# Optimization experiments

Hardware: AMD Instinct MI355X
Metric: run time of the kernel (lower is better)

Reference implementation:

```python
import jax, jax.numpy as jnp
import numpy as np

BLOCK = 128          # quantization block size
F8_MAX = 448.0       # max representable magnitude of float8_e4m3fn


def setup_inputs() -> dict:
    key = jax.random.key(0)
    k1, k2, k3 = jax.random.split(key, 3)
    M, K, N = 8192, 4096, 4096
    Kb, Nb = K // BLOCK, N // BLOCK
    x = jax.random.normal(k1, (M, K), jnp.float32)
    # weight stored as fp8-representable values (simulated with f32 container)
    weight = jax.random.normal(k2, (N, K), jnp.float32)
    # per 128x128-block weight dequant scales (positive, small, like amax/448)
    weight_scale = jax.random.uniform(k3, (Nb, Kb), jnp.float32, 0.5, 1.5) * 0.01
    return {"x": x, "weight": weight, "weight_scale": weight_scale}


def _act_quant(x):
    """fp8_blockwise_act_quant: per-(row, 128-block) scale = amax/448, cast to e4m3."""
    M, K = x.shape
    Kb = K // BLOCK
    xb = x.reshape(M, Kb, BLOCK)
    amax = jnp.max(jnp.abs(xb), axis=-1, keepdims=True)            # [M, Kb, 1]
    scale = jnp.maximum(amax, 1e-12) / F8_MAX                      # [M, Kb, 1]
    xq = (xb / scale).astype(jnp.float8_e4m3fn).astype(jnp.float32)
    return xq, scale


def reference(x, weight, weight_scale):
    # ---- activation blockwise fp8 quant ----
    xq, x_scale = _act_quant(x)                                    # [M,Kb,B], [M,Kb,1]
    M, Kb, _ = xq.shape
    K = Kb * BLOCK
    x_deq = (xq * x_scale).reshape(M, K)                           # dequantized activations

    # ---- weight blockwise fp8 dequant (weight stored as fp8 values) ----
    N = weight.shape[0]
    Nb = N // BLOCK
    wq = weight.astype(jnp.float8_e4m3fn).astype(jnp.float32)      # fp8 storage
    w_deq = (wq.reshape(Nb, BLOCK, Kb, BLOCK)
             * weight_scale[:, None, :, None]).reshape(N, K)

    # ---- scaled GEMM: y = x_deq @ w_deq^T (bias is None) ----
    return x_deq @ w_deq.T                                         # [M, N]
```

## Files before the change

### kernel.cpp

```cpp
#include <hip/hip_runtime.h>


typedef int   v4i __attribute__((ext_vector_type(4)));
typedef int   v8i __attribute__((ext_vector_type(8)));
typedef float v4f __attribute__((ext_vector_type(4)));

constexpr int M  = 8192;
constexpr int K  = 4096;
constexpr int N  = 4096;
constexpr int KB = K / 128;
constexpr int NB = N / 128;

#define GLOBAL_AS __attribute__((address_space(1)))
#define LDS_AS    __attribute__((address_space(3)))

__device__ __forceinline__ void async16(const void* g, void* l) {
  __builtin_amdgcn_global_load_lds((const GLOBAL_AS void*)g, (LDS_AS void*)l, 16, 0, 0);
}


__global__ __launch_bounds__(256) void quant_x_kernel(
    const float* __restrict__ x, unsigned char* __restrict__ xq,
    float* __restrict__ xs_t ) {
  const int tid = threadIdx.x;
  const long long blk = ((long long)blockIdx.x * 256 + tid) >> 3;
  const int s = tid & 7;
  const int m  = (int)(blk >> 5);
  const int kb = (int)(blk & (KB - 1));

  const float4* px = (const float4*)(x + blk * 128 + s * 16);
  float4 v0 = px[0], v1 = px[1], v2 = px[2], v3 = px[3];

  float ax = 0.f;
#define AMAX4(v) ax = fmaxf(ax, fmaxf(fmaxf(fabsf(v.x), fabsf(v.y)), fmaxf(fabsf(v.z), fabsf(v.w))))
  AMAX4(v0); AMAX4(v1); AMAX4(v2); AMAX4(v3);
#undef AMAX4
#pragma unroll
  for (int d = 4; d >= 1; d >>= 1) ax = fmaxf(ax, __shfl_xor(ax, d, 8));
  const float scale = fmaxf(ax, 1e-12f) / 448.0f;

  int p0 = 0, p1 = 0, p2 = 0, p3 = 0;
  p0 = __builtin_amdgcn_cvt_pk_fp8_f32(v0.x / scale, v0.y / scale, p0, false);
  p0 = __builtin_amdgcn_cvt_pk_fp8_f32(v0.z / scale, v0.w / scale, p0, true);
  p1 = __builtin_amdgcn_cvt_pk_fp8_f32(v1.x / scale, v1.y / scale, p1, false);
  p1 = __builtin_amdgcn_cvt_pk_fp8_f32(v1.z / scale, v1.w / scale, p1, true);
  p2 = __builtin_amdgcn_cvt_pk_fp8_f32(v2.x / scale, v2.y / scale, p2, false);
  p2 = __builtin_amdgcn_cvt_pk_fp8_f32(v2.z / scale, v2.w / scale, p2, true);
  p3 = __builtin_amdgcn_cvt_pk_fp8_f32(v3.x / scale, v3.y / scale, p3, false);
  p3 = __builtin_amdgcn_cvt_pk_fp8_f32(v3.z / scale, v3.w / scale, p3, true);

  const int q = s >> 1, j = s & 1, rr = m & 15;
  const long long base = ((long long)(m >> 4) * KB + kb) * 2048;
  *(v4i*)(xq + base + j * 1024 + (q * 16 + rr) * 16) = (v4i){p0, p1, p2, p3};

  if (s == 0) xs_t[(long long)kb * M + m] = scale;
}

__global__ __launch_bounds__(256) void quant_w_kernel(
    const float* __restrict__ w, unsigned char* __restrict__ wq) {
  const long long t = (long long)blockIdx.x * 256 + threadIdx.x;
  const int grp = (int)(t >> 7);
  const int idx = (int)(t & 127);
  const int l = idx >> 1, j = idx & 1;
  const int nf = grp >> 5, kb = grp & (KB - 1);
  const int n = nf * 16 + (l & 15);
  const int k = kb * 128 + (l >> 4) * 32 + j * 16;

  const float4* pw = (const float4*)(w + (long long)n * K + k);
  float4 v0 = pw[0], v1 = pw[1], v2 = pw[2], v3 = pw[3];
  int p0 = 0, p1 = 0, p2 = 0, p3 = 0;
  p0 = __builtin_amdgcn_cvt_pk_fp8_f32(v0.x, v0.y, p0, false);
  p0 = __builtin_amdgcn_cvt_pk_fp8_f32(v0.z, v0.w, p0, true);
  p1 = __builtin_amdgcn_cvt_pk_fp8_f32(v1.x, v1.y, p1, false);
  p1 = __builtin_amdgcn_cvt_pk_fp8_f32(v1.z, v1.w, p1, true);
  p2 = __builtin_amdgcn_cvt_pk_fp8_f32(v2.x, v2.y, p2, false);
  p2 = __builtin_amdgcn_cvt_pk_fp8_f32(v2.z, v2.w, p2, true);
  p3 = __builtin_amdgcn_cvt_pk_fp8_f32(v3.x, v3.y, p3, false);
  p3 = __builtin_amdgcn_cvt_pk_fp8_f32(v3.z, v3.w, p3, true);
  *(v4i*)(wq + (long long)grp * 2048 + j * 1024 + l * 16) = (v4i){p0, p1, p2, p3};
}

__global__ __launch_bounds__(256, 2) void gemm_fp8_kernel(
    const unsigned char* __restrict__ xq, const unsigned char* __restrict__ wq,
    const float* __restrict__ xs_t ,
    const float* __restrict__ wscale ,
    float* __restrict__ out) {
  __shared__ unsigned char Asm[16 * 2048];
  __shared__ unsigned char Bsm[8 * 2048];
  __shared__ float Stab[KB * 256];

  const int tid   = threadIdx.x;
  const int ntile = blockIdx.x;
  const int mtile = blockIdx.y;
  const int wave  = tid >> 6;
  const int lane  = tid & 63;
  const int wm = wave >> 1, wn = wave & 1;
  const int l15 = lane & 15, quad = lane >> 4;

  for (int i = tid; i < KB * 256; i += 256) {
    const int kb = i >> 8, r = i & 255;
    Stab[i] = xs_t[(long long)kb * M + mtile * 256 + r] * wscale[ntile * KB + kb];
  }

  const unsigned char* pa0 =
      xq + ((long long)(mtile * 16 + wave * 4) * KB) * 2048 + lane * 16;
  const unsigned char* pb0 =
      wq + ((long long)(ntile * 8 + wave * 2) * KB) * 2048 + lane * 16;
  const int a_lds0 = wave * 4 * 2048;
  const int b_lds0 = wave * 2 * 2048;

  v4f acc[8][4];
#pragma unroll
  for (int f = 0; f < 8; ++f)
#pragma unroll
    for (int g = 0; g < 4; ++g) acc[f][g] = (v4f){0.f, 0.f, 0.f, 0.f};

  const v4f z = (v4f){0.f, 0.f, 0.f, 0.f};

#pragma unroll 1
  for (int kb = 0; kb < KB; ++kb) {
    const long long koff = (long long)kb * 2048;
#pragma unroll
    for (int t = 0; t < 8; ++t)
      async16(pa0 + koff + (long long)(t >> 1) * (KB * 2048) + (t & 1) * 1024,
              Asm + a_lds0 + (t >> 1) * 2048 + (t & 1) * 1024);
#pragma unroll
    for (int t = 0; t < 4; ++t)
      async16(pb0 + koff + (long long)(t >> 1) * (KB * 2048) + (t & 1) * 1024,
              Bsm + b_lds0 + (t >> 1) * 2048 + (t & 1) * 1024);
    __syncthreads();

    v8i b[4];
#pragma unroll
    for (int g = 0; g < 4; ++g) {
      const unsigned char* pb = Bsm + (wn * 4 + g) * 2048 + lane * 16;
      v4i lo = *(const v4i*)pb;
      v4i hi = *(const v4i*)(pb + 1024);
      b[g][0] = lo[0]; b[g][1] = lo[1]; b[g][2] = lo[2]; b[g][3] = lo[3];
      b[g][4] = hi[0]; b[g][5] = hi[1]; b[g][6] = hi[2]; b[g][7] = hi[3];
    }

#pragma unroll
    for (int f = 0; f < 8; ++f) {
      const unsigned char* pa = Asm + (wm * 8 + f) * 2048 + lane * 16;
      v4i lo = *(const v4i*)pa;
      v4i hi = *(const v4i*)(pa + 1024);
      v8i a;
      a[0] = lo[0]; a[1] = lo[1]; a[2] = lo[2]; a[3] = lo[3];
      a[4] = hi[0]; a[5] = hi[1]; a[6] = hi[2]; a[7] = hi[3];
      const v4f sx = *(const v4f*)(Stab + kb * 256 + wm * 128 + f * 16 + quad * 4);
#pragma unroll
      for (int g = 0; g < 4; ++g) {
        v4f p = __builtin_amdgcn_mfma_scale_f32_16x16x128_f8f6f4(
            a, b[g], z, 0, 0, 0, 0x7f7f7f7f, 0, 0x7f7f7f7f);
        acc[f][g] += sx * p;
      }
    }
    __syncthreads();
  }

#pragma unroll
  for (int f = 0; f < 8; ++f) {
#pragma unroll
    for (int r = 0; r < 4; ++r) {
      const long long row = mtile * 256 + wm * 128 + f * 16 + quad * 4 + r;
      float* po = out + row * N + ntile * 128 + wn * 64 + l15;
#pragma unroll
      for (int g = 0; g < 4; ++g) po[g * 16] = acc[f][g][r];
    }
  }
}

extern "C" void kernel_launch(void* const* d_in, const int* in_sizes, int n_in,
                              void* d_out, int out_size, void* d_ws, size_t ws_size,
                              hipStream_t stream) {
  const float* x   = (const float*)d_in[0];
  const float* w   = (const float*)d_in[1];
  const float* wsc = (const float*)d_in[2];
  float* out = (float*)d_out;

  unsigned char* ws = (unsigned char*)d_ws;
  unsigned char* xq = ws;
  unsigned char* wq = ws + (size_t)M * K;
  float* xs_t = (float*)(ws + (size_t)M * K + (size_t)N * K);

  quant_x_kernel<<<(M * KB * 8) / 256, 256, 0, stream>>>(x, xq, xs_t);
  quant_w_kernel<<<(int)(((long long)N * K / 16) / 256), 256, 0, stream>>>(w, wq);
  gemm_fp8_kernel<<<dim3(NB, M / 256), 256, 0, stream>>>(xq, wq, xs_t, wsc, out);
}
```

Measured before the change: 427.8 us.

## Fuse quant kernels, double-buffer GEMM with 256x256 tiles and 512 threads

Merges the activation and weight quantization kernels into one launch. The GEMM moves to 256x256 output tiles with 8 waves, double-buffers the A and B tiles in LDS, and overlaps the next k-block load with compute using explicit vmcnt waits. It also streams per-k activation scales asynchronously instead of precomputing a full scale table, reads the weight scale via readlane, and raises MFMA issue priority. Each tile now uses more LDS and there are fewer workgroups (512), so occupancy and load balance across CUs may suffer.

Result: no change. 422.9 us (-1.1%).

```diff
diff --git a/kernel.cpp b/kernel.cpp
--- a/kernel.cpp
+++ b/kernel.cpp
@@ -11,6 +11,9 @@
 constexpr int KB = K / 128;
 constexpr int NB = N / 128;
 
+constexpr int XBLOCKS = (M * KB * 8) / 256;
+constexpr int WBLOCKS = (int)(((long long)N * K / 16) / 256);
+
 #define GLOBAL_AS __attribute__((address_space(1)))
 #define LDS_AS    __attribute__((address_space(3)))
 
@@ -19,95 +22,104 @@
 }
 
 
-__global__ __launch_bounds__(256) void quant_x_kernel(
-    const float* __restrict__ x, unsigned char* __restrict__ xq,
+__global__ __launch_bounds__(256) void quant_fused_kernel(
+    const float* __restrict__ x, const float* __restrict__ w,
+    unsigned char* __restrict__ xq, unsigned char* __restrict__ wq,
     float* __restrict__ xs_t ) {
   const int tid = threadIdx.x;
-  const long long blk = ((long long)blockIdx.x * 256 + tid) >> 3;
-  const int s = tid & 7;
-  const int m  = (int)(blk >> 5);
-  const int kb = (int)(blk & (KB - 1));
-
-  const float4* px = (const float4*)(x + blk * 128 + s * 16);
-  float4 v0 = px[0], v1 = px[1], v2 = px[2], v3 = px[3];
-
-  float ax = 0.f;
+  if (blockIdx.x < XBLOCKS) {
+    const long long blk = ((long long)blockIdx.x * 256 + tid) >> 3;
+    const int s = tid & 7;
+    const int m  = (int)(blk >> 5);
+    const int kb = (int)(blk & (KB - 1));
+
+    const float4* px = (const float4*)(x + blk * 128 + s * 16);
+    float4 v0 = px[0], v1 = px[1], v2 = px[2], v3 = px[3];
+
+    float ax = 0.f;
 #define AMAX4(v) ax = fmaxf(ax, fmaxf(fmaxf(fabsf(v.x), fabsf(v.y)), fmaxf(fabsf(v.z), fabsf(v.w))))
-  AMAX4(v0); AMAX4(v1); AMAX4(v2); AMAX4(v3);
+    AMAX4(v0); AMAX4(v1); AMAX4(v2); AMAX4(v3);
 #undef AMAX4
 #pragma unroll
-  for (int d = 4; d >= 1; d >>= 1) ax = fmaxf(ax, __shfl_xor(ax, d, 8));
-  const float scale = fmaxf(ax, 1e-12f) / 448.0f;
-
-  int p0 = 0, p1 = 0, p2 = 0, p3 = 0;
-  p0 = __builtin_amdgcn_cvt_pk_fp8_f32(v0.x / scale, v0.y / scale, p0, false);
-  p0 = __builtin_amdgcn_cvt_pk_fp8_f32(v0.z / scale, v0.w / scale, p0, true);
-  p1 = __builtin_amdgcn_cvt_pk_fp8_f32(v1.x / scale, v1.y / scale, p1, false);
-  p1 = __builtin_amdgcn_cvt_pk_fp8_f32(v1.z / scale, v1.w / scale, p1, true);
-  p2 = __builtin_amdgcn_cvt_pk_fp8_f32(v2.x / scale, v2.y / scale, p2, false);
-  p2 = __builtin_amdgcn_cvt_pk_fp8_f32(v2.z / scale, v2.w / scale, p2, true);
-  p3 = __builtin_amdgcn_cvt_pk_fp8_f32(v3.x / scale, v3.y / scale, p3, false);
-  p3 = __builtin_amdgcn_cvt_pk_fp8_f32(v3.z / scale, v3.w / scale, p3, true);
-
-  const int q = s >> 1, j = s & 1, rr = m & 15;
-  const long long base = ((long long)(m >> 4) * KB + kb) * 2048;
-  *(v4i*)(xq + base + j * 1024 + (q * 16 + rr) * 16) = (v4i){p0, p1, p2, p3};
-
-  if (s == 0) xs_t[(long long)kb * M + m] = scale;
-}
-
-__global__ __launch_bounds__(256) void quant_w_kernel(
-    const float* __restrict__ w, unsigned char* __restrict__ wq) {
-  const long long t = (long long)blockIdx.x * 256 + threadIdx.x;
-  const int grp = (int)(t >> 7);
-  const int idx = (int)(t & 127);
-  const int l = idx >> 1, j = idx & 1;
-  const int nf = grp >> 5, kb = grp & (KB - 1);
-  const int n = nf * 16 + (l & 15);
-  const int k = kb * 128 + (l >> 4) * 32 + j * 16;
-
-  const float4* pw = (const float4*)(w + (long long)n * K + k);
-  float4 v0 = pw[0], v1 = pw[1], v2 = pw[2], v3 = pw[3];
-  int p0 = 0, p1 = 0, p2 = 0, p3 = 0;
-  p0 = __builtin_amdgcn_cvt_pk_fp8_f32(v0.x, v0.y, p0, false);
-  p0 = __builtin_amdgcn_cvt_pk_fp8_f32(v0.z, v0.w, p0, true);
-  p1 = __builtin_amdgcn_cvt_pk_fp8_f32(v1.x, v1.y, p1, false);
-  p1 = __builtin_amdgcn_cvt_pk_fp8_f32(v1.z, v1.w, p1, true);
-  p2 = __builtin_amdgcn_cvt_pk_fp8_f32(v2.x, v2.y, p2, false);
-  p2 = __builtin_amdgcn_cvt_pk_fp8_f32(v2.z, v2.w, p2, true);
-  p3 = __builtin_amdgcn_cvt_pk_fp8_f32(v3.x, v3.y, p3, false);
-  p3 = __builtin_amdgcn_cvt_pk_fp8_f32(v3.z, v3.w, p3, true);
-  *(v4i*)(wq + (long long)grp * 2048 + j * 1024 + l * 16) = (v4i){p0, p1, p2, p3};
-}
-
-__global__ __launch_bounds__(256, 2) void gemm_fp8_kernel(
+    for (int d = 4; d >= 1; d >>= 1) ax = fmaxf(ax, __shfl_xor(ax, d, 8));
+    const float scale = fmaxf(ax, 1e-12f) / 448.0f;
+
+    int p0 = 0, p1 = 0, p2 = 0, p3 = 0;
+    p0 = __builtin_amdgcn_cvt_pk_fp8_f32(v0.x / scale, v0.y / scale, p0, false);
+    p0 = __builtin_amdgcn_cvt_pk_fp8_f32(v0.z / scale, v0.w / scale, p0, true);
+    p1 = __builtin_amdgcn_cvt_pk_fp8_f32(v1.x / scale, v1.y / scale, p1, false);
+    p1 = __builtin_amdgcn_cvt_pk_fp8_f32(v1.z / scale, v1.w / scale, p1, true);
+    p2 = __builtin_amdgcn_cvt_pk_fp8_f32(v2.x / scale, v2.y / scale, p2, false);
+    p2 = __builtin_amdgcn_cvt_pk_fp8_f32(v2.z / scale, v2.w / scale, p2, true);
+    p3 = __builtin_amdgcn_cvt_pk_fp8_f32(v3.x / scale, v3.y / scale, p3, false);
+    p3 = __builtin_amdgcn_cvt_pk_fp8_f32(v3.z / scale, v3.w / scale, p3, true);
+
+    const int q = s >> 1, j = s & 1, rr = m & 15;
+    const long long base = ((long long)(m >> 4) * KB + kb) * 2048;
+    *(v4i*)(xq + base + j * 1024 + (q * 16 + rr) * 16) = (v4i){p0, p1, p2, p3};
+
+    if (s == 0) xs_t[(long long)kb * M + m] = scale;
+  } else {
+    const long long t = (long long)(blockIdx.x - XBLOCKS) * 256 + tid;
+    const int grp = (int)(t >> 7);
+    const int idx = (int)(t & 127);
+    const int l = idx >> 1, j = idx & 1;
+    const int nf = grp >> 5, kb = grp & (KB - 1);
+    const int n = nf * 16 + (l & 15);
+    const int k = kb * 128 + (l >> 4) * 32 + j * 16;
+
+    const float4* pw = (const float4*)(w + (long long)n * K + k);
+    float4 v0 = pw[0], v1 = pw[1], v2 = pw[2], v3 = pw[3];
+    int p0 = 0, p1 = 0, p2 = 0, p3 = 0;
+    p0 = __builtin_amdgcn_cvt_pk_fp8_f32(v0.x, v0.y, p0, false);
+    p0 = __builtin_amdgcn_cvt_pk_fp8_f32(v0.z, v0.w, p0, true);
+    p1 = __builtin_amdgcn_cvt_pk_fp8_f32(v1.x, v1.y, p1, false);
+    p1 = __builtin_amdgcn_cvt_pk_fp8_f32(v1.z, v1.w, p1, true);
+    p2 = __builtin_amdgcn_cvt_pk_fp8_f32(v2.x, v2.y, p2, false);
+    p2 = __builtin_amdgcn_cvt_pk_fp8_f32(v2.z, v2.w, p2, true);
+    p3 = __builtin_amdgcn_cvt_pk_fp8_f32(v3.x, v3.y, p3, false);
+    p3 = __builtin_amdgcn_cvt_pk_fp8_f32(v3.z, v3.w, p3, true);
+    *(v4i*)(wq + (long long)grp * 2048 + j * 1024 + l * 16) = (v4i){p0, p1, p2, p3};
+  }
+}
+
+__global__ __launch_bounds__(512, 2) void gemm_fp8_kernel(
     const unsigned char* __restrict__ xq, const unsigned char* __restrict__ wq,
     const float* __restrict__ xs_t ,
     const float* __restrict__ wscale ,
     float* __restrict__ out) {
-  __shared__ unsigned char Asm[16 * 2048];
-  __shared__ unsigned char Bsm[8 * 2048];
-  __shared__ float Stab[KB * 256];
+  __shared__ unsigned char Asm[2][16 * 2048];
+  __shared__ unsigned char Bsm[2][16 * 2048];
+  __shared__ float Ssm[2][256];
 
   const int tid   = threadIdx.x;
   const int ntile = blockIdx.x;
   const int mtile = blockIdx.y;
   const int wave  = tid >> 6;
   const int lane  = tid & 63;
-  const int wm = wave >> 1, wn = wave & 1;
+  const int wm = wave >> 2, wn = wave & 3;
   const int l15 = lane & 15, quad = lane >> 4;
 
-  for (int i = tid; i < KB * 256; i += 256) {
-    const int kb = i >> 8, r = i & 255;
-    Stab[i] = xs_t[(long long)kb * M + mtile * 256 + r] * wscale[ntile * KB + kb];
-  }
+  const float wsv = wscale[(ntile * 2 + (wn >> 1)) * KB + (lane & 31)];
 
   const unsigned char* pa0 =
-      xq + ((long long)(mtile * 16 + wave * 4) * KB) * 2048 + lane * 16;
+      xq + ((long long)(mtile * 16 + wave * 2) * KB) * 2048 + lane * 16;
   const unsigned char* pb0 =
-      wq + ((long long)(ntile * 8 + wave * 2) * KB) * 2048 + lane * 16;
-  const int a_lds0 = wave * 4 * 2048;
-  const int b_lds0 = wave * 2 * 2048;
+      wq + ((long long)(ntile * 16 + wave * 2) * KB) * 2048 + lane * 16;
+  const char* ps0 = (const char*)(xs_t + (long long)mtile * 256) + lane * 16;
+
+  auto STAGE = [&](int nbuf, int kbi) {
+    const long long koff = (long long)kbi * 2048;
+#pragma unroll
+    for (int t = 0; t < 4; ++t)
+      async16(pa0 + koff + (long long)(t >> 1) * (KB * 2048) + (t & 1) * 1024,
+              &Asm[nbuf][(wave * 2 + (t >> 1)) * 2048 + (t & 1) * 1024]);
+#pragma unroll
+    for (int t = 0; t < 4; ++t)
+      async16(pb0 + koff + (long long)(t >> 1) * (KB * 2048) + (t & 1) * 1024,
+              &Bsm[nbuf][(wave * 2 + (t >> 1)) * 2048 + (t & 1) * 1024]);
+    if (wave == 0) async16(ps0 + (long long)kbi * (M * 4), &Ssm[nbuf][0]);
+  };
 
   v4f acc[8][4];
 #pragma unroll
@@ -116,24 +128,30 @@
     for (int g = 0; g < 4; ++g) acc[f][g] = (v4f){0.f, 0.f, 0.f, 0.f};
 
   const v4f z = (v4f){0.f, 0.f, 0.f, 0.f};
+
+  STAGE(0, 0);
 
 #pragma unroll 1
   for (int kb = 0; kb < KB; ++kb) {
-    const long long koff = (long long)kb * 2048;
-#pragma unroll
-    for (int t = 0; t < 8; ++t)
-      async16(pa0 + koff + (long long)(t >> 1) * (KB * 2048) + (t & 1) * 1024,
-              Asm + a_lds0 + (t >> 1) * 2048 + (t & 1) * 1024);
-#pragma unroll
-    for (int t = 0; t < 4; ++t)
-      async16(pb0 + koff + (long long)(t >> 1) * (KB * 2048) + (t & 1) * 1024,
-              Bsm + b_lds0 + (t >> 1) * 2048 + (t & 1) * 1024);
-    __syncthreads();
+    const int cur = kb & 1;
+    if (kb < KB - 1) {
+      STAGE(cur ^ 1, kb + 1);
+      if (wave == 0) asm volatile("s_waitcnt vmcnt(9)" ::: "memory");
+      else           asm volatile("s_waitcnt vmcnt(8)" ::: "memory");
+    } else {
+      asm volatile("s_waitcnt vmcnt(0)" ::: "memory");
+    }
+    __builtin_amdgcn_s_barrier();
+    asm volatile("" ::: "memory");
+    __builtin_amdgcn_sched_barrier(0);
+
+    const float ws =
+        __uint_as_float(__builtin_amdgcn_readlane(__float_as_uint(wsv), kb));
 
     v8i b[4];
 #pragma unroll
     for (int g = 0; g < 4; ++g) {
-      const unsigned char* pb = Bsm + (wn * 4 + g) * 2048 + lane * 16;
+      const unsigned char* pb = Bsm[cur] + (wn * 4 + g) * 2048 + lane * 16;
       v4i lo = *(const v4i*)pb;
       v4i hi = *(const v4i*)(pb + 1024);
       b[g][0] = lo[0]; b[g][1] = lo[1]; b[g][2] = lo[2]; b[g][3] = lo[3];
@@ -142,19 +160,24 @@
 
 #pragma unroll
     for (int f = 0; f < 8; ++f) {
-      const unsigned char* pa = Asm + (wm * 8 + f) * 2048 + lane * 16;
+      const unsigned char* pa = Asm[cur] + (wm * 8 + f) * 2048 + lane * 16;
       v4i lo = *(const v4i*)pa;
       v4i hi = *(const v4i*)(pa + 1024);
       v8i a;
       a[0] = lo[0]; a[1] = lo[1]; a[2] = lo[2]; a[3] = lo[3];
       a[4] = hi[0]; a[5] = hi[1]; a[6] = hi[2]; a[7] = hi[3];
-      const v4f sx = *(const v4f*)(Stab + kb * 256 + wm * 128 + f * 16 + quad * 4);
+      const v4f sxr = *(const v4f*)&Ssm[cur][wm * 128 + f * 16 + quad * 4];
+      const v4f s = sxr * ws;
+      v4f p[4];
+      __builtin_amdgcn_s_setprio(1);
 #pragma unroll
       for (int g = 0; g < 4; ++g) {
-        v4f p = __builtin_amdgcn_mfma_scale_f32_16x16x128_f8f6f4(
+        p[g] = __builtin_amdgcn_mfma_scale_f32_16x16x128_f8f6f4(
             a, b[g], z, 0, 0, 0, 0x7f7f7f7f, 0, 0x7f7f7f7f);
-        acc[f][g] += sx * p;
       }
+      __builtin_amdgcn_s_setprio(0);
+#pragma unroll
+      for (int g = 0; g < 4; ++g) acc[f][g] += s * p[g];
     }
     __syncthreads();
   }
@@ -164,7 +187,7 @@
 #pragma unroll
     for (int r = 0; r < 4; ++r) {
       const long long row = mtile * 256 + wm * 128 + f * 16 + quad * 4 + r;
-      float* po = out + row * N + ntile * 128 + wn * 64 + l15;
+      float* po = out + row * N + ntile * 256 + wn * 64 + l15;
 #pragma unroll
       for (int g = 0; g < 4; ++g) po[g * 16] = acc[f][g][r];
     }
@@ -184,7 +207,6 @@
   unsigned char* wq = ws + (size_t)M * K;
   float* xs_t = (float*)(ws + (size_t)M * K + (size_t)N * K);
 
-  quant_x_kernel<<<(M * KB * 8) / 256, 256, 0, stream>>>(x, xq, xs_t);
-  quant_w_kernel<<<(int)(((long long)N * K / 16) / 256), 256, 0, stream>>>(w, wq);
-  gemm_fp8_kernel<<<dim3(NB, M / 256), 256, 0, stream>>>(xq, wq, xs_t, wsc, out);
-}
+  quant_fused_kernel<<<XBLOCKS + WBLOCKS, 256, 0, stream>>>(x, w, xq, wq, xs_t);
+  gemm_fp8_kernel<<<dim3(N / 256, M / 256), 512, 0, stream>>>(xq, wq, xs_t, wsc, out);
+}
```
